# Kernel optimization log

Hardware: AMD Instinct MI355X
Metric: run time of the kernel (lower is better)

## Reference

```python
import jax, jax.numpy as jnp
import numpy as np

B, N, IN_F, OUT_F, H = 4, 1024, 256, 256, 8
HID = OUT_F // H  # 32
ALPHA = 0.2  # leaky relu negative slope


def setup_inputs() -> dict:
    key = jax.random.key(0)
    k1, k2, k3, k4 = jax.random.split(key, 4)
    h = jax.random.normal(k1, (B, N, IN_F), dtype=jnp.float32)
    # linear: in_features -> n_heads*n_hidden, no bias (stored as [in, out])
    W = jax.random.normal(k2, (IN_F, H * HID), dtype=jnp.float32) / np.sqrt(IN_F)
    # attn: Linear(2*n_hidden, 1, bias=False), shared across heads
    attn_w = jax.random.normal(k3, (2 * HID,), dtype=jnp.float32) / np.sqrt(2 * HID)
    # random dense adjacency (p=0.5) plus self loops, broadcast over heads
    u = jax.random.uniform(k4, (B, N, N, 1), dtype=jnp.float32)
    adj_mat = jnp.maximum((u < 0.5).astype(jnp.float32), jnp.eye(N, dtype=jnp.float32)[None, :, :, None])
    return {"h": h, "adj_mat": adj_mat, "W": W, "attn_w": attn_w}


def reference(h, adj_mat, W, attn_w):
    # g: [b, n, h, d]
    g = (h @ W).reshape(B, N, H, HID)
    # attn(concat(g_i, g_j)) decomposes: e[b,i,j,h] = <attn_w[:HID], g_i> + <attn_w[HID:], g_j>
    # (exactly the math of the repeat/repeat_interleave/cat + 1-wide linear, without the N^2 concat)
    e_i = jnp.einsum('bnhd,d->bnh', g, attn_w[:HID])   # g_repeat_interleave part (index i)
    e_j = jnp.einsum('bnhd,d->bnh', g, attn_w[HID:])   # g_repeat part (index j)
    e = e_i[:, :, None, :] + e_j[:, None, :, :]        # [b, i, j, h]
    e = jnp.where(e >= 0, e, ALPHA * e)                # LeakyReLU(alpha)
    e = jnp.where(adj_mat == 0, -jnp.inf, e)           # masked_fill
    a = jax.nn.softmax(e, axis=1)                      # faithful: original uses Softmax(dim=1)
    # dropout p acts as identity in eval mode / p=0
    out = jnp.einsum('bijh,bjhd->bihd', a, g)          # [b, i, h, d]
    return out.reshape(B, N, H * HID)                  # is_concat=True
```

## Files before the change

### kernel.cpp

```cpp
#include <hip/hip_runtime.h>
#include <math.h>

#define BB 4
#define NN 1024
#define HH 8
#define NROW (BB*NN)

typedef short s8v __attribute__((ext_vector_type(8)));
typedef float f4v __attribute__((ext_vector_type(4)));

__device__ __forceinline__ float lrelu(float x) { return fmaxf(x, 0.2f * x); }
__device__ __forceinline__ short bf16rne(float f) {
    unsigned u = __float_as_uint(f);
    u += 0x7FFF + ((u >> 16) & 1u);
    return (short)(u >> 16);
}

__global__ __launch_bounds__(256) void k_gemm_ei(const float* __restrict__ hm,
                                                 const float* __restrict__ W,
                                                 const float* __restrict__ aw,
                                                 float* __restrict__ g,
                                                 float* __restrict__ e_i,
                                                 float* __restrict__ e_j,
                                                 float* __restrict__ e_jt) {
    __shared__ __align__(16) float hs[8][256];
    __shared__ float aws[64];
    const int row0 = blockIdx.x * 8;
    const int t = threadIdx.x;
    if (t < 64) aws[t] = aw[t];
    const float4* h4 = (const float4*)(hm + row0 * 256);
    float4* hs4 = (float4*)&hs[0][0];
    hs4[t] = h4[t];
    hs4[t + 256] = h4[t + 256];
    __syncthreads();

    float acc[8];
#pragma unroll
    for (int r = 0; r < 8; ++r) acc[r] = 0.f;
    for (int k4 = 0; k4 < 64; ++k4) {
        const float w0 = W[(4 * k4 + 0) * 256 + t];
        const float w1 = W[(4 * k4 + 1) * 256 + t];
        const float w2 = W[(4 * k4 + 2) * 256 + t];
        const float w3 = W[(4 * k4 + 3) * 256 + t];
#pragma unroll
        for (int r = 0; r < 8; ++r) {
            const float4 hv = *(const float4*)&hs[r][4 * k4];
            acc[r] = fmaf(hv.x, w0, acc[r]);
            acc[r] = fmaf(hv.y, w1, acc[r]);
            acc[r] = fmaf(hv.z, w2, acc[r]);
            acc[r] = fmaf(hv.w, w3, acc[r]);
        }
    }
    const int d = t & 31, hh = t >> 5;
    const int b = row0 >> 10;
#pragma unroll
    for (int r = 0; r < 8; ++r) {
        g[(row0 + r) * 256 + t] = acc[r];
        float vi = acc[r] * aws[d];
        float vj = acc[r] * aws[32 + d];
#pragma unroll
        for (int mm = 1; mm < 32; mm <<= 1) {
            vi += __shfl_xor(vi, mm);
            vj += __shfl_xor(vj, mm);
        }
        if (d == 0) {
            e_i[(row0 + r) * 8 + hh] = vi;
            e_j[(row0 + r) * 8 + hh] = vj;
            e_jt[(size_t)(b * 8 + hh) * NN + ((row0 + r) & (NN - 1))] = vj;
        }
    }
}

__global__ __launch_bounds__(256) void k_s(const float* __restrict__ adj,
                                           const float* __restrict__ e_i,
                                           const float* __restrict__ e_j,
                                           float* __restrict__ ps) {
    __shared__ __align__(16) float eis[128 * 8];
    __shared__ float ejs[8][64];
    __shared__ float sp[4][8][64];
    const int bx = blockIdx.x;
    const int b = bx >> 7, jc = (bx >> 3) & 15, ic = bx & 7;
    const int j0 = jc * 64, i0 = ic * 128;
    const int t = threadIdx.x;

    ((float4*)eis)[t] = ((const float4*)(e_i + (b * NN + i0) * 8))[t];
    if (t < 128) {
        const float4 v = ((const float4*)(e_j + (b * NN + j0) * 8))[t];
        const int base = t * 4;
        ejs[(base + 0) & 7][(base + 0) >> 3] = v.x;
        ejs[(base + 1) & 7][(base + 1) >> 3] = v.y;
        ejs[(base + 2) & 7][(base + 2) >> 3] = v.z;
        ejs[(base + 3) & 7][(base + 3) >> 3] = v.w;
    }
    __syncthreads();

    const int ii = t >> 6, jj = t & 63;
    float ejv[8], sacc[8];
#pragma unroll
    for (int h = 0; h < 8; ++h) { ejv[h] = ejs[h][jj]; sacc[h] = 0.f; }
    const float* adjp = adj + (size_t)b * NN * NN + j0 + jj;
    for (int i = ii; i < 128; i += 4) {
        const float a = adjp[(size_t)(i0 + i) * NN];
        const float* ep = &eis[i * 8];
#pragma unroll
        for (int h = 0; h < 8; ++h)
            sacc[h] = fmaf(a, __expf(lrelu(ep[h] + ejv[h])), sacc[h]);
    }
#pragma unroll
    for (int h = 0; h < 8; ++h) sp[ii][h][jj] = sacc[h];
    __syncthreads();
#pragma unroll
    for (int k = 0; k < 2; ++k) {
        const int idx = t * 2 + k;
        const int jjo = idx >> 3, h = idx & 7;
        const float s = sp[0][h][jjo] + sp[1][h][jjo] + sp[2][h][jjo] + sp[3][h][jjo];
        ps[ic * (NROW * 8) + (b * NN + j0 + jjo) * 8 + h] = s;
    }
}

__global__ __launch_bounds__(256) void k_prep(const float* __restrict__ ps,
                                              const float* __restrict__ g,
                                              short* __restrict__ Gt) {
    __shared__ float rss[16][8];
    const int bx = blockIdx.x;
    const int b = bx >> 6, j0 = (bx & 63) * 16;
    const int t = threadIdx.x;
    if (t < 128) {
        const int jj = t >> 3, h = t & 7;
        float s = 0.f;
#pragma unroll
        for (int ic = 0; ic < 8; ++ic)
            s += ps[ic * (NROW * 8) + (b * NN + j0 + jj) * 8 + h];
        rss[jj][h] = 1.0f / s;
    }
    __syncthreads();
    const int h = t >> 5, d = t & 31;
    unsigned short v16[16];
#pragma unroll
    for (int r = 0; r < 16; ++r) {
        const float val = g[(size_t)(b * NN + j0 + r) * 256 + t] * rss[r][h];
        v16[r] = (unsigned short)bf16rne(val);
    }
    const int jt = j0 >> 5, jj0 = j0 & 31;
    short* dst = Gt + ((size_t)((b * 8 + h) * 32 + jt)) * 1024 + d * 32 + jj0;
    uint4 w0, w1;
    w0.x = (unsigned)v16[0] | ((unsigned)v16[1] << 16);
    w0.y = (unsigned)v16[2] | ((unsigned)v16[3] << 16);
    w0.z = (unsigned)v16[4] | ((unsigned)v16[5] << 16);
    w0.w = (unsigned)v16[6] | ((unsigned)v16[7] << 16);
    w1.x = (unsigned)v16[8] | ((unsigned)v16[9] << 16);
    w1.y = (unsigned)v16[10] | ((unsigned)v16[11] << 16);
    w1.z = (unsigned)v16[12] | ((unsigned)v16[13] << 16);
    w1.w = (unsigned)v16[14] | ((unsigned)v16[15] << 16);
    *(uint4*)dst = w0;
    *(uint4*)(dst + 8) = w1;
}

__global__ __launch_bounds__(256) void k_out_mfma(const float* __restrict__ adj,
                                                  const short* __restrict__ Gt,
                                                  const float* __restrict__ e_i,
                                                  const float* __restrict__ e_jt,
                                                  float* __restrict__ out) {
    __shared__ short gts[4][4][32][40];
    __shared__ float ejt[4][128];
    const int bx = blockIdx.x;
    const int hs = bx >> 8, b = (bx >> 6) & 3, i0 = (bx & 63) * 16;
    const int t = threadIdx.x;
    const int wave = t >> 6, lane = t & 63;
    const int m = lane & 15, q = lane >> 4;
    const int h = hs * 4 + wave;

    const float ei = e_i[(size_t)(b * NN + i0 + m) * 8 + h];
    f4v acc0 = {0.f, 0.f, 0.f, 0.f}, acc1 = {0.f, 0.f, 0.f, 0.f};

    const float* adjrow = adj + (size_t)b * NN * NN + (size_t)(i0 + m) * NN;
    const float4* gtg4 = (const float4*)Gt;
    const float4* ejt4 = (const float4*)(e_jt + (size_t)b * 8 * NN);

    for (int s = 0; s < 8; ++s) {
        float4 g0, g1, g2, g3, g4, g5, g6, g7;
#define LG(k)                                                                     \
        {                                                                         \
            const int u = t + 256 * (k);                                          \
            g##k = gtg4[(size_t)(b * 8 + hs * 4 + (u >> 9)) * 4096 + s * 512 +    \
                        (u & 511)];                                               \
        }
        LG(0) LG(1) LG(2) LG(3) LG(4) LG(5) LG(6) LG(7)
#undef LG
        f4v a0, a1, a2, a3, a4, a5, a6, a7;
#define LA(k2, lt, half)                                                          \
        a##k2 = *(const f4v*)&adjrow[s * 128 + (lt) * 32 + q * 8 + (half) * 4];
        LA(0, 0, 0) LA(1, 0, 1) LA(2, 1, 0) LA(3, 1, 1)
        LA(4, 2, 0) LA(5, 2, 1) LA(6, 3, 0) LA(7, 3, 1)
#undef LA
        float4 ev = make_float4(0.f, 0.f, 0.f, 0.f);
        if (t < 128) ev = ejt4[(size_t)(hs * 4 + (t >> 5)) * 256 + s * 32 + (t & 31)];
        __syncthreads();
#define SG(k)                                                                     \
        {                                                                         \
            const int u = t + 256 * (k);                                          \
            char* dstp = (char*)gts + (u >> 9) * 10240 + ((u >> 7) & 3) * 2560 +  \
                         ((u >> 2) & 31) * 80 + (u & 3) * 16;                     \
            *(float4*)dstp = g##k;                                                \
        }
        SG(0) SG(1) SG(2) SG(3) SG(4) SG(5) SG(6) SG(7)
#undef SG
        if (t < 128) *(float4*)&ejt[t >> 5][(t & 31) * 4] = ev;
        __syncthreads();

#define LT(lt, aA, aB)                                                            \
        {                                                                         \
            const f4v ej0 = *(const f4v*)&ejt[wave][(lt) * 32 + q * 8];           \
            const f4v ej1 = *(const f4v*)&ejt[wave][(lt) * 32 + q * 8 + 4];       \
            s8v A;                                                                \
            A[0] = bf16rne(aA[0] * __expf(lrelu(ei + ej0[0])));                   \
            A[1] = bf16rne(aA[1] * __expf(lrelu(ei + ej0[1])));                   \
            A[2] = bf16rne(aA[2] * __expf(lrelu(ei + ej0[2])));                   \
            A[3] = bf16rne(aA[3] * __expf(lrelu(ei + ej0[3])));                   \
            A[4] = bf16rne(aB[0] * __expf(lrelu(ei + ej1[0])));                   \
            A[5] = bf16rne(aB[1] * __expf(lrelu(ei + ej1[1])));                   \
            A[6] = bf16rne(aB[2] * __expf(lrelu(ei + ej1[2])));                   \
            A[7] = bf16rne(aB[3] * __expf(lrelu(ei + ej1[3])));                   \
            const s8v B0 = *(const s8v*)&gts[wave][lt][m][q * 8];                 \
            const s8v B1 = *(const s8v*)&gts[wave][lt][m + 16][q * 8];            \
            acc0 = __builtin_amdgcn_mfma_f32_16x16x32_bf16(A, B0, acc0, 0, 0, 0); \
            acc1 = __builtin_amdgcn_mfma_f32_16x16x32_bf16(A, B1, acc1, 0, 0, 0); \
        }
        LT(0, a0, a1) LT(1, a2, a3) LT(2, a4, a5) LT(3, a6, a7)
#undef LT
    }

    float* op = out + (size_t)(b * NN + i0) * 256;
#pragma unroll
    for (int r = 0; r < 4; ++r) {
        const int row = q * 4 + r;
        op[(size_t)row * 256 + h * 32 + m] = acc0[r];
        op[(size_t)row * 256 + h * 32 + 16 + m] = acc1[r];
    }
}

extern "C" void kernel_launch(void* const* d_in, const int* in_sizes, int n_in,
                              void* d_out, int out_size, void* d_ws, size_t ws_size,
                              hipStream_t stream) {
    const float* h      = (const float*)d_in[0];
    const float* adj    = (const float*)d_in[1];
    const float* W      = (const float*)d_in[2];
    const float* attn_w = (const float*)d_in[3];
    float* out = (float*)d_out;

    float* ws = (float*)d_ws;
    float* g    = ws;
    float* e_i  = g + NROW * 256;
    float* e_j  = e_i + NROW * 8;
    float* e_jt = e_j + NROW * 8;
    float* ps   = e_jt + NROW * 8;
    short* Gt   = (short*)(ps + 8 * NROW * 8);

    k_gemm_ei<<<NROW / 8, 256, 0, stream>>>(h, W, attn_w, g, e_i, e_j, e_jt);
    k_s<<<512, 256, 0, stream>>>(adj, e_i, e_j, ps);
    k_prep<<<256, 256, 0, stream>>>(ps, g, Gt);
    k_out_mfma<<<512, 256, 0, stream>>>(adj, Gt, e_i, e_jt, out);
}
```

Measured before the change: 122.7 us.

## Factor exp(leakyrelu(ei+ej)) into precomputed exponentials, drop per-pair exp

Uses exp(lrelu(x)) = max(exp(x), exp(0.2x)) together with the separability of exp(ei+ej). Each node's exp(e) and exp(0.2e) are precomputed once in the GEMM kernel, so the N^2 attention passes compute two multiplies and a max instead of an add, a leaky relu and a transcendental exp per element. The MFMA kernel also switches to the packed v_cvt_pk_bf16_f32 instruction for bf16 conversion. This risks overflow or underflow for large |e| because the factored exponentials are not max-stabilised, and it doubles the per-node auxiliary storage.

```diff
diff --git a/kernel.cpp b/kernel.cpp
--- a/kernel.cpp
+++ b/kernel.cpp
@@ -9,7 +9,6 @@
 typedef short s8v __attribute__((ext_vector_type(8)));
 typedef float f4v __attribute__((ext_vector_type(4)));
 
-__device__ __forceinline__ float lrelu(float x) { return fmaxf(x, 0.2f * x); }
 __device__ __forceinline__ short bf16rne(float f) {
     unsigned u = __float_as_uint(f);
     u += 0x7FFF + ((u >> 16) & 1u);
@@ -20,9 +19,9 @@
                                                  const float* __restrict__ W,
                                                  const float* __restrict__ aw,
                                                  float* __restrict__ g,
-                                                 float* __restrict__ e_i,
-                                                 float* __restrict__ e_j,
-                                                 float* __restrict__ e_jt) {
+                                                 float* __restrict__ EFi,
+                                                 float* __restrict__ EFj,
+                                                 float* __restrict__ EFjt) {
     __shared__ __align__(16) float hs[8][256];
     __shared__ float aws[64];
     const int row0 = blockIdx.x * 8;
@@ -64,50 +63,65 @@
             vj += __shfl_xor(vj, mm);
         }
         if (d == 0) {
-            e_i[(row0 + r) * 8 + hh] = vi;
-            e_j[(row0 + r) * 8 + hh] = vj;
-            e_jt[(size_t)(b * 8 + hh) * NN + ((row0 + r) & (NN - 1))] = vj;
+            const int row = row0 + r;
+            const float Ei = __expf(vi), Fi = __expf(0.2f * vi);
+            const float Ej = __expf(vj), Fj = __expf(0.2f * vj);
+            *(float2*)&EFi[(size_t)row * 16 + hh * 2] = make_float2(Ei, Fi);
+            *(float2*)&EFj[(size_t)row * 16 + hh * 2] = make_float2(Ej, Fj);
+            const int n = row & (NN - 1);
+            EFjt[((size_t)(b * 8 + hh) * 2 + 0) * NN + n] = Ej;
+            EFjt[((size_t)(b * 8 + hh) * 2 + 1) * NN + n] = Fj;
         }
     }
 }
 
 __global__ __launch_bounds__(256) void k_s(const float* __restrict__ adj,
-                                           const float* __restrict__ e_i,
-                                           const float* __restrict__ e_j,
+                                           const float* __restrict__ EFi,
+                                           const float* __restrict__ EFj,
                                            float* __restrict__ ps) {
-    __shared__ __align__(16) float eis[128 * 8];
-    __shared__ float ejs[8][64];
+    __shared__ __align__(16) float eis[128 * 16];
     __shared__ float sp[4][8][64];
     const int bx = blockIdx.x;
     const int b = bx >> 7, jc = (bx >> 3) & 15, ic = bx & 7;
     const int j0 = jc * 64, i0 = ic * 128;
     const int t = threadIdx.x;
 
-    ((float4*)eis)[t] = ((const float4*)(e_i + (b * NN + i0) * 8))[t];
-    if (t < 128) {
-        const float4 v = ((const float4*)(e_j + (b * NN + j0) * 8))[t];
-        const int base = t * 4;
-        ejs[(base + 0) & 7][(base + 0) >> 3] = v.x;
-        ejs[(base + 1) & 7][(base + 1) >> 3] = v.y;
-        ejs[(base + 2) & 7][(base + 2) >> 3] = v.z;
-        ejs[(base + 3) & 7][(base + 3) >> 3] = v.w;
-    }
-    __syncthreads();
+    const float4* src4 = (const float4*)(EFi + (size_t)(b * NN + i0) * 16);
+    ((float4*)eis)[t] = src4[t];
+    ((float4*)eis)[t + 256] = src4[t + 256];
 
     const int ii = t >> 6, jj = t & 63;
-    float ejv[8], sacc[8];
-#pragma unroll
-    for (int h = 0; h < 8; ++h) { ejv[h] = ejs[h][jj]; sacc[h] = 0.f; }
+    const float* ej = EFj + (size_t)(b * NN + j0 + jj) * 16;
+    const float4 f0 = *(const float4*)&ej[0];
+    const float4 f1 = *(const float4*)&ej[4];
+    const float4 f2 = *(const float4*)&ej[8];
+    const float4 f3 = *(const float4*)&ej[12];
+    const float ejE0 = f0.x, ejF0 = f0.y, ejE1 = f0.z, ejF1 = f0.w;
+    const float ejE2 = f1.x, ejF2 = f1.y, ejE3 = f1.z, ejF3 = f1.w;
+    const float ejE4 = f2.x, ejF4 = f2.y, ejE5 = f2.z, ejF5 = f2.w;
+    const float ejE6 = f3.x, ejF6 = f3.y, ejE7 = f3.z, ejF7 = f3.w;
+    __syncthreads();
+
+    float s0 = 0.f, s1 = 0.f, s2 = 0.f, s3 = 0.f;
+    float s4 = 0.f, s5 = 0.f, s6 = 0.f, s7 = 0.f;
     const float* adjp = adj + (size_t)b * NN * NN + j0 + jj;
     for (int i = ii; i < 128; i += 4) {
         const float a = adjp[(size_t)(i0 + i) * NN];
-        const float* ep = &eis[i * 8];
-#pragma unroll
-        for (int h = 0; h < 8; ++h)
-            sacc[h] = fmaf(a, __expf(lrelu(ep[h] + ejv[h])), sacc[h]);
-    }
-#pragma unroll
-    for (int h = 0; h < 8; ++h) sp[ii][h][jj] = sacc[h];
+        const float4 x0 = *(const float4*)&eis[i * 16];
+        const float4 x1 = *(const float4*)&eis[i * 16 + 4];
+        const float4 x2 = *(const float4*)&eis[i * 16 + 8];
+        const float4 x3 = *(const float4*)&eis[i * 16 + 12];
+        s0 = fmaf(a, fmaxf(x0.x * ejE0, x0.y * ejF0), s0);
+        s1 = fmaf(a, fmaxf(x0.z * ejE1, x0.w * ejF1), s1);
+        s2 = fmaf(a, fmaxf(x1.x * ejE2, x1.y * ejF2), s2);
+        s3 = fmaf(a, fmaxf(x1.z * ejE3, x1.w * ejF3), s3);
+        s4 = fmaf(a, fmaxf(x2.x * ejE4, x2.y * ejF4), s4);
+        s5 = fmaf(a, fmaxf(x2.z * ejE5, x2.w * ejF5), s5);
+        s6 = fmaf(a, fmaxf(x3.x * ejE6, x3.y * ejF6), s6);
+        s7 = fmaf(a, fmaxf(x3.z * ejE7, x3.w * ejF7), s7);
+    }
+    sp[ii][0][jj] = s0; sp[ii][1][jj] = s1; sp[ii][2][jj] = s2; sp[ii][3][jj] = s3;
+    sp[ii][4][jj] = s4; sp[ii][5][jj] = s5; sp[ii][6][jj] = s6; sp[ii][7][jj] = s7;
     __syncthreads();
 #pragma unroll
     for (int k = 0; k < 2; ++k) {
@@ -158,11 +172,11 @@
 
 __global__ __launch_bounds__(256) void k_out_mfma(const float* __restrict__ adj,
                                                   const short* __restrict__ Gt,
-                                                  const float* __restrict__ e_i,
-                                                  const float* __restrict__ e_jt,
+                                                  const float* __restrict__ EFi,
+                                                  const float* __restrict__ EFjt,
                                                   float* __restrict__ out) {
     __shared__ short gts[4][4][32][40];
-    __shared__ float ejt[4][128];
+    __shared__ float ejt[4][2][128];
     const int bx = blockIdx.x;
     const int hs = bx >> 8, b = (bx >> 6) & 3, i0 = (bx & 63) * 16;
     const int t = threadIdx.x;
@@ -170,12 +184,13 @@
     const int m = lane & 15, q = lane >> 4;
     const int h = hs * 4 + wave;
 
-    const float ei = e_i[(size_t)(b * NN + i0 + m) * 8 + h];
+    const float2 eif = *(const float2*)&EFi[(size_t)(b * NN + i0 + m) * 16 + h * 2];
+    const float EiV = eif.x, FiV = eif.y;
     f4v acc0 = {0.f, 0.f, 0.f, 0.f}, acc1 = {0.f, 0.f, 0.f, 0.f};
 
     const float* adjrow = adj + (size_t)b * NN * NN + (size_t)(i0 + m) * NN;
     const float4* gtg4 = (const float4*)Gt;
-    const float4* ejt4 = (const float4*)(e_jt + (size_t)b * 8 * NN);
+    const float4* ejt4 = (const float4*)(EFjt + (size_t)b * 8 * 2 * NN);
 
     for (int s = 0; s < 8; ++s) {
         float4 g0, g1, g2, g3, g4, g5, g6, g7;
@@ -193,8 +208,9 @@
         LA(0, 0, 0) LA(1, 0, 1) LA(2, 1, 0) LA(3, 1, 1)
         LA(4, 2, 0) LA(5, 2, 1) LA(6, 3, 0) LA(7, 3, 1)
 #undef LA
-        float4 ev = make_float4(0.f, 0.f, 0.f, 0.f);
-        if (t < 128) ev = ejt4[(size_t)(hs * 4 + (t >> 5)) * 256 + s * 32 + (t & 31)];
+        const float4 ev =
+            ejt4[(size_t)((hs * 4 + (t >> 6)) * 2 + ((t >> 5) & 1)) * 256 +
+                 s * 32 + (t & 31)];
         __syncthreads();
 #define SG(k)                                                                     \
         {                                                                         \
@@ -205,22 +221,31 @@
         }
         SG(0) SG(1) SG(2) SG(3) SG(4) SG(5) SG(6) SG(7)
 #undef SG
-        if (t < 128) *(float4*)&ejt[t >> 5][(t & 31) * 4] = ev;
+        *(float4*)&ejt[t >> 6][(t >> 5) & 1][(t & 31) * 4] = ev;
         __syncthreads();
 
 #define LT(lt, aA, aB)                                                            \
         {                                                                         \
-            const f4v ej0 = *(const f4v*)&ejt[wave][(lt) * 32 + q * 8];           \
-            const f4v ej1 = *(const f4v*)&ejt[wave][(lt) * 32 + q * 8 + 4];       \
-            s8v A;                                                                \
-            A[0] = bf16rne(aA[0] * __expf(lrelu(ei + ej0[0])));                   \
-            A[1] = bf16rne(aA[1] * __expf(lrelu(ei + ej0[1])));                   \
-            A[2] = bf16rne(aA[2] * __expf(lrelu(ei + ej0[2])));                   \
-            A[3] = bf16rne(aA[3] * __expf(lrelu(ei + ej0[3])));                   \
-            A[4] = bf16rne(aB[0] * __expf(lrelu(ei + ej1[0])));                   \
-            A[5] = bf16rne(aB[1] * __expf(lrelu(ei + ej1[1])));                   \
-            A[6] = bf16rne(aB[2] * __expf(lrelu(ei + ej1[2])));                   \
-            A[7] = bf16rne(aB[3] * __expf(lrelu(ei + ej1[3])));                   \
+            const f4v ejA = *(const f4v*)&ejt[wave][0][(lt) * 32 + q * 8];        \
+            const f4v ejB = *(const f4v*)&ejt[wave][0][(lt) * 32 + q * 8 + 4];    \
+            const f4v fjA = *(const f4v*)&ejt[wave][1][(lt) * 32 + q * 8];        \
+            const f4v fjB = *(const f4v*)&ejt[wave][1][(lt) * 32 + q * 8 + 4];    \
+            const float p0 = aA[0] * fmaxf(EiV * ejA[0], FiV * fjA[0]);           \
+            const float p1 = aA[1] * fmaxf(EiV * ejA[1], FiV * fjA[1]);           \
+            const float p2 = aA[2] * fmaxf(EiV * ejA[2], FiV * fjA[2]);           \
+            const float p3 = aA[3] * fmaxf(EiV * ejA[3], FiV * fjA[3]);           \
+            const float p4 = aB[0] * fmaxf(EiV * ejB[0], FiV * fjB[0]);           \
+            const float p5 = aB[1] * fmaxf(EiV * ejB[1], FiV * fjB[1]);           \
+            const float p6 = aB[2] * fmaxf(EiV * ejB[2], FiV * fjB[2]);           \
+            const float p7 = aB[3] * fmaxf(EiV * ejB[3], FiV * fjB[3]);           \
+            unsigned w0, w1, w2, w3;                                              \
+            asm("v_cvt_pk_bf16_f32 %0, %1, %2" : "=v"(w0) : "v"(p0), "v"(p1));    \
+            asm("v_cvt_pk_bf16_f32 %0, %1, %2" : "=v"(w1) : "v"(p2), "v"(p3));    \
+            asm("v_cvt_pk_bf16_f32 %0, %1, %2" : "=v"(w2) : "v"(p4), "v"(p5));    \
+            asm("v_cvt_pk_bf16_f32 %0, %1, %2" : "=v"(w3) : "v"(p6), "v"(p7));    \
+            union { unsigned u[4]; s8v v; } Au;                                   \
+            Au.u[0] = w0; Au.u[1] = w1; Au.u[2] = w2; Au.u[3] = w3;               \
+            const s8v A = Au.v;                                                   \
             const s8v B0 = *(const s8v*)&gts[wave][lt][m][q * 8];                 \
             const s8v B1 = *(const s8v*)&gts[wave][lt][m + 16][q * 8];            \
             acc0 = __builtin_amdgcn_mfma_f32_16x16x32_bf16(A, B0, acc0, 0, 0, 0); \
@@ -250,14 +275,14 @@
 
     float* ws = (float*)d_ws;
     float* g    = ws;
-    float* e_i  = g + NROW * 256;
-    float* e_j  = e_i + NROW * 8;
-    float* e_jt = e_j + NROW * 8;
-    float* ps   = e_jt + NROW * 8;
+    float* EFi  = g + NROW * 256;
+    float* EFj  = EFi + NROW * 16;
+    float* EFjt = EFj + NROW * 16;
+    float* ps   = EFjt + NROW * 16;
     short* Gt   = (short*)(ps + 8 * NROW * 8);
 
-    k_gemm_ei<<<NROW / 8, 256, 0, stream>>>(h, W, attn_w, g, e_i, e_j, e_jt);
-    k_s<<<512, 256, 0, stream>>>(adj, e_i, e_j, ps);
+    k_gemm_ei<<<NROW / 8, 256, 0, stream>>>(h, W, attn_w, g, EFi, EFj, EFjt);
+    k_s<<<512, 256, 0, stream>>>(adj, EFi, EFj, ps);
     k_prep<<<256, 256, 0, stream>>>(ps, g, Gt);
-    k_out_mfma<<<512, 256, 0, stream>>>(adj, Gt, e_i, e_jt, out);
-}
+    k_out_mfma<<<512, 256, 0, stream>>>(adj, Gt, EFi, EFjt, out);
+}
```

After: 124.4 us. About the same (+1.4%).
